# Kernel tuning notes

Measured on AMD Instinct MI355X. Metric: run time of the kernel, lower is better.

The kernel has to match this reference:

```python
import jax, jax.numpy as jnp
import numpy as np

B, C, N, OUT, K = 8, 64, 4096, 64, 20
KNN_SKIP = 6   # knn computed on channels 6: (as in x[:, 6:])
BN_EPS = 1e-5
NEG_SLOPE = 0.2


def setup_inputs() -> dict:
    key = jax.random.key(0)
    k1, k2, k3, k4 = jax.random.split(key, 4)
    x = jax.random.normal(k1, (B, C, N), dtype=jnp.float32)
    W = jax.random.normal(k2, (OUT, 2 * C), dtype=jnp.float32) * (1.0 / np.sqrt(2 * C))
    gamma = jax.random.normal(k3, (OUT,), dtype=jnp.float32) * 0.1 + 1.0
    beta = jax.random.normal(k4, (OUT,), dtype=jnp.float32) * 0.1
    return {"x": x, "W": W, "gamma": gamma, "beta": beta}


def _knn_idx(xk, k):
    # xk: (B, Ck, N). pairwise_distance[b,i,j] = -||x_i - x_j||^2
    sq = jnp.sum(xk * xk, axis=1)                       # (B, N)
    inner = jnp.einsum('bcn,bcm->bnm', xk, xk)          # (B, N, N)
    pd = 2.0 * inner - sq[:, :, None] - sq[:, None, :]  # (B, N, N)
    return jax.lax.top_k(pd, k)[1]                      # (B, N, k) int32


def reference(x, W, gamma, beta):
    idx = _knn_idx(x[:, KNN_SKIP:, :], K)               # (B, N, K)
    xt = jnp.transpose(x, (0, 2, 1))                    # (B, N, C)
    # gather neighbor features: (B, N, K, C)
    neigh = jnp.take_along_axis(xt[:, None, :, :], idx[:, :, :, None], axis=2)
    center = jnp.broadcast_to(xt[:, :, None, :], neigh.shape)
    edge = jnp.concatenate([neigh - center, center], axis=-1)  # (B, N, K, 2C)
    # 1x1 conv (no bias): contract channel dim -> (B, OUT, N, K)
    y = jnp.einsum('bnkc,oc->bonk', edge, W)
    # BatchNorm2d (training-mode batch stats, biased variance)
    mean = jnp.mean(y, axis=(0, 2, 3), keepdims=True)
    var = jnp.var(y, axis=(0, 2, 3), keepdims=True)
    y = (y - mean) * jax.lax.rsqrt(var + BN_EPS)
    y = y * gamma[None, :, None, None] + beta[None, :, None, None]
    # LeakyReLU(0.2)
    y = jnp.where(y >= 0, y, NEG_SLOPE * y)
    # max over k neighbors -> (B, OUT, N)
    return jnp.max(y, axis=-1)
```

## Files before the change

kernel.cpp:

```cpp
#include <hip/hip_runtime.h>
#include <cstdint>
#include <cstddef>

#define BB 8
#define CC 64
#define NN 4096
#define OO 64
#define KK 20
#define KC 58
#define HC 29
#define KSKIP 6
#define NSPLIT 8
#define JS 512
#define TIDX 8
#define REC 28
#define BN_EPS 1e-5f
#define NEG 0.2f
#define NEGINF (-3.402823466e38f)
#define M_TOTAL 655360.0f
#define HPAD 4

#define MED3F(a, b, c) __builtin_amdgcn_fmed3f((a), (b), (c))


__global__ void k_sq(const float* __restrict__ x, float* __restrict__ h) {
  int n = blockIdx.x * 256 + threadIdx.x;
  int b = n >> 12;
  int nn = n & (NN - 1);
  const float* xp = x + ((size_t)b * CC + KSKIP) * NN + nn;
  float s = 0.f;
#pragma unroll
  for (int c = 0; c < KC; ++c) {
    float v = xp[(size_t)c * NN];
    s = fmaf(v, v, s);
  }
  h[n] = 0.5f * s;
}

#define RIP(tv, e)                                   \
  do {                                               \
    float _e = (e);                                  \
    tv[19] = MED3F(tv[18], tv[19], _e);              \
    tv[18] = MED3F(tv[17], tv[18], _e);              \
    tv[17] = MED3F(tv[16], tv[17], _e);              \
    tv[16] = MED3F(tv[15], tv[16], _e);              \
    tv[15] = MED3F(tv[14], tv[15], _e);              \
    tv[14] = MED3F(tv[13], tv[14], _e);              \
    tv[13] = MED3F(tv[12], tv[13], _e);              \
    tv[12] = MED3F(tv[11], tv[12], _e);              \
    tv[11] = MED3F(tv[10], tv[11], _e);              \
    tv[10] = MED3F(tv[9],  tv[10], _e);              \
    tv[9]  = MED3F(tv[8],  tv[9],  _e);              \
    tv[8]  = MED3F(tv[7],  tv[8],  _e);              \
    tv[7]  = MED3F(tv[6],  tv[7],  _e);              \
    tv[6]  = MED3F(tv[5],  tv[6],  _e);              \
    tv[5]  = MED3F(tv[4],  tv[5],  _e);              \
    tv[4]  = MED3F(tv[3],  tv[4],  _e);              \
    tv[3]  = MED3F(tv[2],  tv[3],  _e);              \
    tv[2]  = MED3F(tv[1],  tv[2],  _e);              \
    tv[1]  = MED3F(tv[0],  tv[1],  _e);              \
    tv[0]  = fmaxf(tv[0], _e);                       \
  } while (0)

#define RIPX(tv, ti, e, jj)                                                   \
  do {                                                                        \
    float _e = (e);                                                           \
    int _j = (jj);                                                            \
    bool c0 = _e > tv[0], c1 = _e > tv[1], c2 = _e > tv[2], c3 = _e > tv[3];  \
    bool c4 = _e > tv[4], c5 = _e > tv[5], c6 = _e > tv[6], c7 = _e > tv[7];  \
    tv[19] = MED3F(tv[18], tv[19], _e);                                       \
    tv[18] = MED3F(tv[17], tv[18], _e);                                       \
    tv[17] = MED3F(tv[16], tv[17], _e);                                       \
    tv[16] = MED3F(tv[15], tv[16], _e);                                       \
    tv[15] = MED3F(tv[14], tv[15], _e);                                       \
    tv[14] = MED3F(tv[13], tv[14], _e);                                       \
    tv[13] = MED3F(tv[12], tv[13], _e);                                       \
    tv[12] = MED3F(tv[11], tv[12], _e);                                       \
    tv[11] = MED3F(tv[10], tv[11], _e);                                       \
    tv[10] = MED3F(tv[9],  tv[10], _e);                                       \
    tv[9]  = MED3F(tv[8],  tv[9],  _e);                                       \
    tv[8]  = MED3F(tv[7],  tv[8],  _e);                                       \
    tv[7]  = MED3F(tv[6],  tv[7],  _e); ti[7] = c6 ? ti[6] : (c7 ? _j : ti[7]); \
    tv[6]  = MED3F(tv[5],  tv[6],  _e); ti[6] = c5 ? ti[5] : (c6 ? _j : ti[6]); \
    tv[5]  = MED3F(tv[4],  tv[5],  _e); ti[5] = c4 ? ti[4] : (c5 ? _j : ti[5]); \
    tv[4]  = MED3F(tv[3],  tv[4],  _e); ti[4] = c3 ? ti[3] : (c4 ? _j : ti[4]); \
    tv[3]  = MED3F(tv[2],  tv[3],  _e); ti[3] = c2 ? ti[2] : (c3 ? _j : ti[3]); \
    tv[2]  = MED3F(tv[1],  tv[2],  _e); ti[2] = c1 ? ti[1] : (c2 ? _j : ti[2]); \
    tv[1]  = MED3F(tv[0],  tv[1],  _e); ti[1] = c0 ? ti[0] : (c1 ? _j : ti[1]); \
    tv[0]  = fmaxf(tv[0], _e);          ti[0] = c0 ? _j : ti[0];              \
  } while (0)

#define DIST8P(jq)                                                    \
  float a0 = 0.f, a1 = 0.f, a2 = 0.f, a3 = 0.f;                       \
  float a4 = 0.f, a5 = 0.f, a6 = 0.f, a7 = 0.f;                       \
  _Pragma("unroll")                                                   \
  for (int cc = 0; cc < HC; ++cc) {                                   \
    float4 x0 = *(const float4*)(ltp + cc * 64 + (jq) * 8);           \
    float4 x1 = *(const float4*)(ltp + cc * 64 + (jq) * 8 + 4);       \
    float xic = xi[cc];                                               \
    a0 = fmaf(xic, x0.x, a0); a1 = fmaf(xic, x0.y, a1);               \
    a2 = fmaf(xic, x0.z, a2); a3 = fmaf(xic, x0.w, a3);               \
    a4 = fmaf(xic, x1.x, a4); a5 = fmaf(xic, x1.y, a5);               \
    a6 = fmaf(xic, x1.z, a6); a7 = fmaf(xic, x1.w, a7);               \
  }                                                                   \
  a0 += __shfl_xor(a0, 1); a1 += __shfl_xor(a1, 1);                   \
  a2 += __shfl_xor(a2, 1); a3 += __shfl_xor(a3, 1);                   \
  a4 += __shfl_xor(a4, 1); a5 += __shfl_xor(a5, 1);                   \
  a6 += __shfl_xor(a6, 1); a7 += __shfl_xor(a7, 1);                   \
  float4 hA = *(const float4*)(lh + (jq) * 8 + half4);                \
  float d0 = (half4 ? a4 : a0) - hA.x;                                \
  float d1 = (half4 ? a5 : a1) - hA.y;                                \
  float d2 = (half4 ? a6 : a2) - hA.z;                                \
  float d3 = (half4 ? a7 : a3) - hA.w;

#define STAGE_TILE(jbase)                                             \
  __syncthreads();                                                    \
  for (int f = t; f < KC * 16; f += 256) {                            \
    int c = f >> 4, q = f & 15;                                       \
    float4 v = *(const float4*)(xb + c * NN + (jbase) + q * 4);       \
    *(float4*)(ltile + c * 64 + q * 4 + (c >= HC ? HPAD : 0)) = v;    \
  }                                                                   \
  if (t < 64) lh[t] = hg[b * NN + (jbase) + t];                       \
  __syncthreads();

__global__ __launch_bounds__(256, 4) void k_knnA(const float* __restrict__ x,
                                                 const float* __restrict__ hg,
                                                 float* __restrict__ candvx) {
  __shared__ float ltile[KC * 64 + HPAD];
  __shared__ float lh[64];
  int t = threadIdx.x;
  int l = t & 63;
  int w = t >> 6;
  int half = l & 1;
  int half4 = half * 4;
  int bidx = blockIdx.x;
  int b = bidx >> 8;
  int itile = (bidx >> 3) & 31;
  int split = bidx & 7;
  int i = itile * 128 + w * 32 + (l >> 1);
  const float* xb = x + ((size_t)b * CC + KSKIP) * NN;
  const float* ltp = ltile + half * (HC * 64 + HPAD);

  float xi[HC];
#pragma unroll
  for (int cc = 0; cc < HC; ++cc) xi[cc] = xb[(half * HC + cc) * NN + i];

  float tv[KK];
  int ti[TIDX];
#pragma unroll
  for (int s = 0; s < KK; ++s) tv[s] = NEGINF;
#pragma unroll
  for (int s = 0; s < TIDX; ++s) ti[s] = -1;

#pragma unroll 1
  for (int jt = 0; jt < JS / 64; ++jt) {
    int jbase = split * JS + jt * 64;
    STAGE_TILE(jbase)
#pragma unroll 1
    for (int jq = 0; jq < 8; ++jq) {
      DIST8P(jq)
      int j0 = jbase + jq * 8 + half4;
      RIPX(tv, ti, d0, j0 + 0); RIPX(tv, ti, d1, j0 + 1);
      RIPX(tv, ti, d2, j0 + 2); RIPX(tv, ti, d3, j0 + 3);
    }
  }

  float ov[KK];
  int oi[TIDX];
#pragma unroll
  for (int s = 0; s < KK; ++s) ov[s] = __shfl_xor(tv[s], 1);
#pragma unroll
  for (int s = 0; s < TIDX; ++s) oi[s] = __shfl_xor(ti[s], 1);
#pragma unroll
  for (int s = 0; s < TIDX; ++s) { RIPX(tv, ti, ov[s], oi[s]); }
#pragma unroll
  for (int s = TIDX; s < KK; ++s) { RIPX(tv, ti, ov[s], -1); }

  if (!half) {
    float* cv = candvx + (((size_t)(b * NN + i)) * NSPLIT + split) * REC;
    *(float4*)(cv + 0)  = make_float4(tv[0], tv[1], tv[2], tv[3]);
    *(float4*)(cv + 4)  = make_float4(tv[4], tv[5], tv[6], tv[7]);
    *(float4*)(cv + 8)  = make_float4(tv[8], tv[9], tv[10], tv[11]);
    *(float4*)(cv + 12) = make_float4(tv[12], tv[13], tv[14], tv[15]);
    *(float4*)(cv + 16) = make_float4(tv[16], tv[17], tv[18], tv[19]);
    int* cvi = (int*)(cv + KK);
    *(int4*)(cvi + 0) = make_int4(ti[0], ti[1], ti[2], ti[3]);
    *(int4*)(cvi + 4) = make_int4(ti[4], ti[5], ti[6], ti[7]);
  }
}

__global__ void k_thresh(const float* __restrict__ candvx, float* __restrict__ thr) {
  int qi = blockIdx.x * 256 + threadIdx.x;
  const float* cv = candvx + (size_t)qi * NSPLIT * REC;
  float tv[KK];
#pragma unroll
  for (int s = 0; s < KK; ++s) tv[s] = NEGINF;
#pragma unroll 1
  for (int sp = 0; sp < NSPLIT; ++sp) {
#pragma unroll
    for (int s = 0; s < KK; ++s) {
      RIP(tv, cv[sp * REC + s]);
    }
  }
  thr[qi] = tv[19];
}

__global__ void k_final(const float* __restrict__ candvx, const float* __restrict__ thr,
                        int* __restrict__ idxk, int* __restrict__ fbl,
                        int* __restrict__ fbcnt) {
  int qi = blockIdx.x * 256 + threadIdx.x;
  float ti_ = thr[qi];
  const float* cv = candvx + (size_t)qi * NSPLIT * REC;
  int* op = idxk + (size_t)qi * KK;
  bool fb = false;
  int m = 0;
#pragma unroll 1
  for (int sp = 0; sp < NSPLIT; ++sp) {
    const float* r = cv + sp * REC;
    if (r[TIDX] >= ti_) fb = true;
    const int* ri = (const int*)(r + KK);
#pragma unroll
    for (int s = 0; s < TIDX; ++s) {
      float v = r[s];
      if (v >= ti_ && ri[s] < 0) fb = true;
      if (v > ti_) {
        if (m < KK) op[m] = ri[s];
        ++m;
      }
    }
  }
  if (m >= KK) fb = true;
  if (fb) {
    int p = atomicAdd(fbcnt, 1);
    fbl[p] = qi;
    return;
  }
  int need = KK - m;
  int last = -1;
#pragma unroll 1
  for (int r2 = 0; r2 < need; ++r2) {
    int best = 0x7fffffff;
#pragma unroll 1
    for (int sp = 0; sp < NSPLIT; ++sp) {
      const float* r = cv + sp * REC;
      const int* ri = (const int*)(r + KK);
#pragma unroll
      for (int s = 0; s < TIDX; ++s) {
        if (r[s] == ti_) {
          int jx = ri[s];
          if (jx > last && jx < best) best = jx;
        }
      }
    }
    op[m + r2] = best;
    last = best;
  }
}

__global__ __launch_bounds__(256) void k_fb(const float* __restrict__ x,
                                            const float* __restrict__ hg,
                                            const float* __restrict__ thr,
                                            const int* __restrict__ fbl,
                                            const int* __restrict__ fbcnt,
                                            int* __restrict__ idxk) {
  __shared__ float xiA[HC];
  __shared__ float xiB[HC];
  __shared__ float db[64 * 2];
  __shared__ int cnt;
  int t = threadIdx.x;
  int nfb = *fbcnt;
  if (nfb > BB * NN) nfb = BB * NN;
#pragma unroll 1
  for (int q = blockIdx.x; q < nfb; q += gridDim.x) {
    int qi = fbl[q];
    int b = qi >> 12;
    int i = qi & (NN - 1);
    const float* xb = x + ((size_t)b * CC + KSKIP) * NN;
    if (t < HC) xiA[t] = xb[t * NN + i];
    else if (t < 2 * HC) xiB[t - HC] = xb[(size_t)t * NN + i];
    if (t == 0) cnt = 0;
    __syncthreads();
    float ti_ = thr[qi];
#pragma unroll 1
    for (int j = t; j < NN; j += 256) {
      float s1 = 0.f, s2 = 0.f;
#pragma unroll
      for (int cc = 0; cc < HC; ++cc) s1 = fmaf(xiA[cc], xb[cc * NN + j], s1);
#pragma unroll
      for (int cc = 0; cc < HC; ++cc) s2 = fmaf(xiB[cc], xb[(HC + cc) * NN + j], s2);
      float d = (s1 + s2) - hg[b * NN + j];
      if (d >= ti_) {
        int p = atomicAdd(&cnt, 1);
        if (p < 64) { db[p * 2] = d; db[p * 2 + 1] = __int_as_float(j); }
      }
    }
    __syncthreads();
    if (t == 0) {
      int n = cnt;
      if (n > 64) n = 64;
      int* op = idxk + (size_t)qi * KK;
      int m = 0;
      for (int e = 0; e < n; ++e) {
        if (db[e * 2] > ti_) {
          if (m < KK) op[m] = __float_as_int(db[e * 2 + 1]);
          ++m;
        }
      }
      int need = KK - m;
      int last = -1;
      for (int r = 0; r < need; ++r) {
        int best = 0x7fffffff;
        for (int e = 0; e < n; ++e) {
          if (db[e * 2] == ti_) {
            int jx = __float_as_int(db[e * 2 + 1]);
            if (jx > last && jx < best) best = jx;
          }
        }
        op[m + r] = best;
        last = best;
      }
    }
    __syncthreads();
  }
}

__global__ void k_uv(const float* __restrict__ x, const float* __restrict__ W,
                     float* __restrict__ ut, float* __restrict__ vt) {
  __shared__ float w1[64 * 65];
  __shared__ float wd[64 * 65];
  __shared__ float xs[64 * 72];
  int t = threadIdx.x;
  int b = blockIdx.x >> 6;
  int nbase = (blockIdx.x & 63) * 64;

  for (int f = t; f < 4096; f += 256) {
    int o = f >> 6, c = f & 63;
    float a = W[o * 128 + c];
    float b2 = W[o * 128 + 64 + c];
    w1[c * 65 + o] = a;
    wd[c * 65 + o] = b2 - a;
  }
  for (int f = t; f < 1024; f += 256) {
    int c = f >> 4, q = f & 15;
    float4 v = *(const float4*)(x + ((size_t)b * CC + c) * NN + nbase + q * 4);
    *(float4*)(xs + c * 72 + q * 4) = v;
  }
  __syncthreads();

  int o = t & 63, w = t >> 6;
  float4 au[4], av[4];
#pragma unroll
  for (int nq = 0; nq < 4; ++nq) {
    au[nq] = make_float4(0.f, 0.f, 0.f, 0.f);
    av[nq] = make_float4(0.f, 0.f, 0.f, 0.f);
  }
#pragma unroll 4
  for (int c = 0; c < 64; ++c) {
    float w1v = w1[c * 65 + o];
    float wdv = wd[c * 65 + o];
#pragma unroll
    for (int nq = 0; nq < 4; ++nq) {
      float4 xv = *(const float4*)(xs + c * 72 + w * 16 + nq * 4);
      au[nq].x = fmaf(w1v, xv.x, au[nq].x);
      au[nq].y = fmaf(w1v, xv.y, au[nq].y);
      au[nq].z = fmaf(w1v, xv.z, au[nq].z);
      au[nq].w = fmaf(w1v, xv.w, au[nq].w);
      av[nq].x = fmaf(wdv, xv.x, av[nq].x);
      av[nq].y = fmaf(wdv, xv.y, av[nq].y);
      av[nq].z = fmaf(wdv, xv.z, av[nq].z);
      av[nq].w = fmaf(wdv, xv.w, av[nq].w);
    }
  }
#pragma unroll
  for (int nq = 0; nq < 4; ++nq) {
    int n = nbase + w * 16 + nq * 4;
    size_t base = ((size_t)b * NN + n) * OO + o;
    ut[base + 0 * OO] = au[nq].x;
    ut[base + 1 * OO] = au[nq].y;
    ut[base + 2 * OO] = au[nq].z;
    ut[base + 3 * OO] = au[nq].w;
    vt[base + 0 * OO] = av[nq].x;
    vt[base + 1 * OO] = av[nq].y;
    vt[base + 2 * OO] = av[nq].z;
    vt[base + 3 * OO] = av[nq].w;
  }
}

__global__ void k_stats(const float* __restrict__ ut, const float* __restrict__ vt,
                        const int* __restrict__ idxk, float* __restrict__ gsum,
                        float* __restrict__ gsqs) {
  __shared__ float red[2][4][64];
  int t = threadIdx.x;
  int o = t & 63, w = t >> 6;
  int b = blockIdx.x >> 6;
  int nbase = (blockIdx.x & 63) * 64 + w * 16;
  const float* up = ut + (size_t)b * NN * OO;
  float s = 0.f, s2 = 0.f;
#pragma unroll 1
  for (int nn2 = 0; nn2 < 16; ++nn2) {
    int n = nbase + nn2;
    float vv = vt[((size_t)b * NN + n) * OO + o];
    const int* ip = idxk + ((size_t)b * NN + n) * KK;
    int4 q0 = *(const int4*)(ip + 0);
    int4 q1 = *(const int4*)(ip + 4);
    int4 q2 = *(const int4*)(ip + 8);
    int4 q3 = *(const int4*)(ip + 12);
    int4 q4 = *(const int4*)(ip + 16);
#define ACC(j)                                  \
    {                                           \
      float u = up[(size_t)(j) * OO + o];       \
      float yy = u + vv;                        \
      s += yy;                                  \
      s2 = fmaf(yy, yy, s2);                    \
    }
    ACC(q0.x) ACC(q0.y) ACC(q0.z) ACC(q0.w)
    ACC(q1.x) ACC(q1.y) ACC(q1.z) ACC(q1.w)
    ACC(q2.x) ACC(q2.y) ACC(q2.z) ACC(q2.w)
    ACC(q3.x) ACC(q3.y) ACC(q3.z) ACC(q3.w)
    ACC(q4.x) ACC(q4.y) ACC(q4.z) ACC(q4.w)
#undef ACC
  }
  red[0][w][o] = s;
  red[1][w][o] = s2;
  __syncthreads();
  if (w == 0) {
    float ts = red[0][0][o] + red[0][1][o] + red[0][2][o] + red[0][3][o];
    float t2 = red[1][0][o] + red[1][1][o] + red[1][2][o] + red[1][3][o];
    atomicAdd(&gsum[o], ts);
    atomicAdd(&gsqs[o], t2);
  }
}

__global__ void k_bn(const float* __restrict__ gsum, const float* __restrict__ gsqs,
                     const float* __restrict__ gamma, const float* __restrict__ beta,
                     float* __restrict__ AB) {
  int o = threadIdx.x;
  float mean = gsum[o] * (1.f / M_TOTAL);
  float var = gsqs[o] * (1.f / M_TOTAL) - mean * mean;
  float A = gamma[o] / sqrtf(var + BN_EPS);
  AB[o] = A;
  AB[64 + o] = beta[o] - mean * A;
}

__global__ void k_out(const float* __restrict__ ut, const float* __restrict__ vt,
                      const int* __restrict__ idxk, const float* __restrict__ AB,
                      float* __restrict__ outp) {
  __shared__ float lt[64 * 65];
  int t = threadIdx.x;
  int o = t & 63, w = t >> 6;
  int b = blockIdx.x >> 6;
  int nb = (blockIdx.x & 63) * 64;
  float A = AB[o], Bs = AB[64 + o];
  const float* up = ut + (size_t)b * NN * OO;
#pragma unroll 1
  for (int nn2 = 0; nn2 < 16; ++nn2) {
    int nl = w * 16 + nn2;
    int n = nb + nl;
    float vv = vt[((size_t)b * NN + n) * OO + o];
    const int* ip = idxk + ((size_t)b * NN + n) * KK;
    int4 q0 = *(const int4*)(ip + 0);
    int4 q1 = *(const int4*)(ip + 4);
    int4 q2 = *(const int4*)(ip + 8);
    int4 q3 = *(const int4*)(ip + 12);
    int4 q4 = *(const int4*)(ip + 16);
    float m = NEGINF;
#define STEP(j)                                   \
    {                                             \
      float u = up[(size_t)(j) * OO + o];         \
      float y = fmaf(A, u + vv, Bs);              \
      y = fmaxf(y, NEG * y);                      \
      m = fmaxf(m, y);                            \
    }
    STEP(q0.x) STEP(q0.y) STEP(q0.z) STEP(q0.w)
    STEP(q1.x) STEP(q1.y) STEP(q1.z) STEP(q1.w)
    STEP(q2.x) STEP(q2.y) STEP(q2.z) STEP(q2.w)
    STEP(q3.x) STEP(q3.y) STEP(q3.z) STEP(q3.w)
    STEP(q4.x) STEP(q4.y) STEP(q4.z) STEP(q4.w)
#undef STEP
    lt[nl * 65 + o] = m;
  }
  __syncthreads();
  int oo = t >> 2, part = t & 3;
#pragma unroll
  for (int mq = 0; mq < 4; ++mq) {
    int n0 = part * 16 + mq * 4;
    float4 vvv;
    vvv.x = lt[(n0 + 0) * 65 + oo];
    vvv.y = lt[(n0 + 1) * 65 + oo];
    vvv.z = lt[(n0 + 2) * 65 + oo];
    vvv.w = lt[(n0 + 3) * 65 + oo];
    *(float4*)(outp + ((size_t)b * OO + oo) * NN + nb + n0) = vvv;
  }
}

extern "C" void kernel_launch(void* const* d_in, const int* in_sizes, int n_in,
                              void* d_out, int out_size, void* d_ws, size_t ws_size,
                              hipStream_t stream) {
  const float* x = (const float*)d_in[0];
  const float* W = (const float*)d_in[1];
  const float* gamma = (const float*)d_in[2];
  const float* beta = (const float*)d_in[3];
  float* outp = (float*)d_out;
  char* ws = (char*)d_ws;

  const size_t NQ = (size_t)BB * NN;
  size_t off = 0;
  float* hg = (float*)(ws + off); off += NQ * 4;
  float* thr = (float*)(ws + off); off += NQ * 4;
  int* idxk = (int*)(ws + off); off += NQ * KK * 4;
  int* fbcnt = (int*)(ws + off); off += 256;
  int* fbl = (int*)(ws + off); off += NQ * 4;
  float* gsum = (float*)(ws + off); off += 256;
  float* gsqs = (float*)(ws + off); off += 256;
  float* AB = (float*)(ws + off); off += 512;
  char* region = ws + off;
  float* candvx = (float*)region;
  float* ut = (float*)region;
  float* vt = (float*)(region + NQ * OO * 4);

  k_sq<<<BB * NN / 256, 256, 0, stream>>>(x, hg);
  k_knnA<<<BB * 32 * NSPLIT, 256, 0, stream>>>(x, hg, candvx);
  k_thresh<<<BB * NN / 256, 256, 0, stream>>>(candvx, thr);
  hipMemsetAsync(fbcnt, 0, 4, stream);
  k_final<<<BB * NN / 256, 256, 0, stream>>>(candvx, thr, idxk, fbl, fbcnt);
  k_fb<<<256, 256, 0, stream>>>(x, hg, thr, fbl, fbcnt, idxk);
  k_uv<<<BB * 64, 256, 0, stream>>>(x, W, ut, vt);
  hipMemsetAsync(gsum, 0, 512, stream);
  k_stats<<<BB * 64, 256, 0, stream>>>(ut, vt, idxk, gsum, gsqs);
  k_bn<<<1, 64, 0, stream>>>(gsum, gsqs, gamma, beta, AB);
  k_out<<<BB * 64, 256, 0, stream>>>(ut, vt, idxk, AB, outp);
}
```

Measured before the change: 691.8 us.

## Track only top-8 per split in knn pass and recompute exact threshold in fallback

The per-split top-K register list in the main knn kernel shrinks from 20 values to 8, cutting the sorting-network work per candidate and halving the candidate record size. The threshold and final kernels are merged: the 20th-best value is estimated from the 8 stored per split, and a query goes to fallback whenever any split's 8th value reaches that threshold. The fallback kernel now computes the exact 20th-best distance itself, using a per-thread top-20 and a shared-memory tree reduction, before collecting neighbours. This trades a cheaper main pass for a possibly much larger fallback rate, since queries whose true neighbours cluster in one split will need a full rescan.

```diff
diff --git a/kernel.cpp b/kernel.cpp
--- a/kernel.cpp
+++ b/kernel.cpp
@@ -13,7 +13,8 @@
 #define NSPLIT 8
 #define JS 512
 #define TIDX 8
-#define REC 28
+#define REC 16
+#define FBCAP 96
 #define BN_EPS 1e-5f
 #define NEG 0.2f
 #define NEGINF (-3.402823466e38f)
@@ -62,32 +63,20 @@
     tv[0]  = fmaxf(tv[0], _e);                       \
   } while (0)
 
-#define RIPX(tv, ti, e, jj)                                                   \
+#define RIPX8(tv, ti, e, jj)                                                  \
   do {                                                                        \
     float _e = (e);                                                           \
     int _j = (jj);                                                            \
     bool c0 = _e > tv[0], c1 = _e > tv[1], c2 = _e > tv[2], c3 = _e > tv[3];  \
     bool c4 = _e > tv[4], c5 = _e > tv[5], c6 = _e > tv[6], c7 = _e > tv[7];  \
-    tv[19] = MED3F(tv[18], tv[19], _e);                                       \
-    tv[18] = MED3F(tv[17], tv[18], _e);                                       \
-    tv[17] = MED3F(tv[16], tv[17], _e);                                       \
-    tv[16] = MED3F(tv[15], tv[16], _e);                                       \
-    tv[15] = MED3F(tv[14], tv[15], _e);                                       \
-    tv[14] = MED3F(tv[13], tv[14], _e);                                       \
-    tv[13] = MED3F(tv[12], tv[13], _e);                                       \
-    tv[12] = MED3F(tv[11], tv[12], _e);                                       \
-    tv[11] = MED3F(tv[10], tv[11], _e);                                       \
-    tv[10] = MED3F(tv[9],  tv[10], _e);                                       \
-    tv[9]  = MED3F(tv[8],  tv[9],  _e);                                       \
-    tv[8]  = MED3F(tv[7],  tv[8],  _e);                                       \
-    tv[7]  = MED3F(tv[6],  tv[7],  _e); ti[7] = c6 ? ti[6] : (c7 ? _j : ti[7]); \
-    tv[6]  = MED3F(tv[5],  tv[6],  _e); ti[6] = c5 ? ti[5] : (c6 ? _j : ti[6]); \
-    tv[5]  = MED3F(tv[4],  tv[5],  _e); ti[5] = c4 ? ti[4] : (c5 ? _j : ti[5]); \
-    tv[4]  = MED3F(tv[3],  tv[4],  _e); ti[4] = c3 ? ti[3] : (c4 ? _j : ti[4]); \
-    tv[3]  = MED3F(tv[2],  tv[3],  _e); ti[3] = c2 ? ti[2] : (c3 ? _j : ti[3]); \
-    tv[2]  = MED3F(tv[1],  tv[2],  _e); ti[2] = c1 ? ti[1] : (c2 ? _j : ti[2]); \
-    tv[1]  = MED3F(tv[0],  tv[1],  _e); ti[1] = c0 ? ti[0] : (c1 ? _j : ti[1]); \
-    tv[0]  = fmaxf(tv[0], _e);          ti[0] = c0 ? _j : ti[0];              \
+    tv[7] = MED3F(tv[6], tv[7], _e); ti[7] = c6 ? ti[6] : (c7 ? _j : ti[7]);  \
+    tv[6] = MED3F(tv[5], tv[6], _e); ti[6] = c5 ? ti[5] : (c6 ? _j : ti[6]);  \
+    tv[5] = MED3F(tv[4], tv[5], _e); ti[5] = c4 ? ti[4] : (c5 ? _j : ti[5]);  \
+    tv[4] = MED3F(tv[3], tv[4], _e); ti[4] = c3 ? ti[3] : (c4 ? _j : ti[4]);  \
+    tv[3] = MED3F(tv[2], tv[3], _e); ti[3] = c2 ? ti[2] : (c3 ? _j : ti[3]);  \
+    tv[2] = MED3F(tv[1], tv[2], _e); ti[2] = c1 ? ti[1] : (c2 ? _j : ti[2]);  \
+    tv[1] = MED3F(tv[0], tv[1], _e); ti[1] = c0 ? ti[0] : (c1 ? _j : ti[1]);  \
+    tv[0] = fmaxf(tv[0], _e);        ti[0] = c0 ? _j : ti[0];                 \
   } while (0)
 
 #define DIST8P(jq)                                                    \
@@ -145,12 +134,10 @@
 #pragma unroll
   for (int cc = 0; cc < HC; ++cc) xi[cc] = xb[(half * HC + cc) * NN + i];
 
-  float tv[KK];
+  float tv[TIDX];
   int ti[TIDX];
 #pragma unroll
-  for (int s = 0; s < KK; ++s) tv[s] = NEGINF;
-#pragma unroll
-  for (int s = 0; s < TIDX; ++s) ti[s] = -1;
+  for (int s = 0; s < TIDX; ++s) { tv[s] = NEGINF; ti[s] = -1; }
 
 #pragma unroll 1
   for (int jt = 0; jt < JS / 64; ++jt) {
@@ -160,76 +147,65 @@
     for (int jq = 0; jq < 8; ++jq) {
       DIST8P(jq)
       int j0 = jbase + jq * 8 + half4;
-      RIPX(tv, ti, d0, j0 + 0); RIPX(tv, ti, d1, j0 + 1);
-      RIPX(tv, ti, d2, j0 + 2); RIPX(tv, ti, d3, j0 + 3);
-    }
-  }
-
-  float ov[KK];
+      RIPX8(tv, ti, d0, j0 + 0); RIPX8(tv, ti, d1, j0 + 1);
+      RIPX8(tv, ti, d2, j0 + 2); RIPX8(tv, ti, d3, j0 + 3);
+    }
+  }
+
+  float ov[TIDX];
   int oi[TIDX];
 #pragma unroll
-  for (int s = 0; s < KK; ++s) ov[s] = __shfl_xor(tv[s], 1);
+  for (int s = 0; s < TIDX; ++s) ov[s] = __shfl_xor(tv[s], 1);
 #pragma unroll
   for (int s = 0; s < TIDX; ++s) oi[s] = __shfl_xor(ti[s], 1);
 #pragma unroll
-  for (int s = 0; s < TIDX; ++s) { RIPX(tv, ti, ov[s], oi[s]); }
-#pragma unroll
-  for (int s = TIDX; s < KK; ++s) { RIPX(tv, ti, ov[s], -1); }
+  for (int s = 0; s < TIDX; ++s) { RIPX8(tv, ti, ov[s], oi[s]); }
 
   if (!half) {
     float* cv = candvx + (((size_t)(b * NN + i)) * NSPLIT + split) * REC;
-    *(float4*)(cv + 0)  = make_float4(tv[0], tv[1], tv[2], tv[3]);
-    *(float4*)(cv + 4)  = make_float4(tv[4], tv[5], tv[6], tv[7]);
-    *(float4*)(cv + 8)  = make_float4(tv[8], tv[9], tv[10], tv[11]);
-    *(float4*)(cv + 12) = make_float4(tv[12], tv[13], tv[14], tv[15]);
-    *(float4*)(cv + 16) = make_float4(tv[16], tv[17], tv[18], tv[19]);
-    int* cvi = (int*)(cv + KK);
+    *(float4*)(cv + 0) = make_float4(tv[0], tv[1], tv[2], tv[3]);
+    *(float4*)(cv + 4) = make_float4(tv[4], tv[5], tv[6], tv[7]);
+    int* cvi = (int*)(cv + TIDX);
     *(int4*)(cvi + 0) = make_int4(ti[0], ti[1], ti[2], ti[3]);
     *(int4*)(cvi + 4) = make_int4(ti[4], ti[5], ti[6], ti[7]);
   }
 }
 
-__global__ void k_thresh(const float* __restrict__ candvx, float* __restrict__ thr) {
+__global__ void k_final(const float* __restrict__ candvx, int* __restrict__ idxk,
+                        int* __restrict__ fbl, int* __restrict__ fbcnt) {
   int qi = blockIdx.x * 256 + threadIdx.x;
   const float* cv = candvx + (size_t)qi * NSPLIT * REC;
   float tv[KK];
 #pragma unroll
   for (int s = 0; s < KK; ++s) tv[s] = NEGINF;
-#pragma unroll 1
-  for (int sp = 0; sp < NSPLIT; ++sp) {
-#pragma unroll
-    for (int s = 0; s < KK; ++s) {
-      RIP(tv, cv[sp * REC + s]);
-    }
-  }
-  thr[qi] = tv[19];
-}
-
-__global__ void k_final(const float* __restrict__ candvx, const float* __restrict__ thr,
-                        int* __restrict__ idxk, int* __restrict__ fbl,
-                        int* __restrict__ fbcnt) {
-  int qi = blockIdx.x * 256 + threadIdx.x;
-  float ti_ = thr[qi];
-  const float* cv = candvx + (size_t)qi * NSPLIT * REC;
-  int* op = idxk + (size_t)qi * KK;
-  bool fb = false;
-  int m = 0;
+  float v7max = NEGINF;
 #pragma unroll 1
   for (int sp = 0; sp < NSPLIT; ++sp) {
     const float* r = cv + sp * REC;
-    if (r[TIDX] >= ti_) fb = true;
-    const int* ri = (const int*)(r + KK);
-#pragma unroll
-    for (int s = 0; s < TIDX; ++s) {
-      float v = r[s];
-      if (v >= ti_ && ri[s] < 0) fb = true;
-      if (v > ti_) {
-        if (m < KK) op[m] = ri[s];
-        ++m;
+#pragma unroll
+    for (int s = 0; s < TIDX; ++s) { RIP(tv, r[s]); }
+    v7max = fmaxf(v7max, r[TIDX - 1]);
+  }
+  float thr = tv[19];
+  int* op = idxk + (size_t)qi * KK;
+  int m = 0;
+  bool fb = (v7max >= thr);
+  if (!fb) {
+#pragma unroll 1
+    for (int sp = 0; sp < NSPLIT; ++sp) {
+      const float* r = cv + sp * REC;
+      const int* ri = (const int*)(r + TIDX);
+#pragma unroll
+      for (int s = 0; s < TIDX; ++s) {
+        float v = r[s];
+        if (v > thr) {
+          if (m < KK) op[m] = ri[s];
+          ++m;
+        }
       }
     }
-  }
-  if (m >= KK) fb = true;
+    if (m >= KK) fb = true;
+  }
   if (fb) {
     int p = atomicAdd(fbcnt, 1);
     fbl[p] = qi;
@@ -243,10 +219,10 @@
 #pragma unroll 1
     for (int sp = 0; sp < NSPLIT; ++sp) {
       const float* r = cv + sp * REC;
-      const int* ri = (const int*)(r + KK);
+      const int* ri = (const int*)(r + TIDX);
 #pragma unroll
       for (int s = 0; s < TIDX; ++s) {
-        if (r[s] == ti_) {
+        if (r[s] == thr) {
           int jx = ri[s];
           if (jx > last && jx < best) best = jx;
         }
@@ -259,13 +235,13 @@
 
 __global__ __launch_bounds__(256) void k_fb(const float* __restrict__ x,
                                             const float* __restrict__ hg,
-                                            const float* __restrict__ thr,
                                             const int* __restrict__ fbl,
                                             const int* __restrict__ fbcnt,
                                             int* __restrict__ idxk) {
   __shared__ float xiA[HC];
   __shared__ float xiB[HC];
-  __shared__ float db[64 * 2];
+  __shared__ float lists[256 * KK];
+  __shared__ float db[FBCAP * 2];
   __shared__ int cnt;
   int t = threadIdx.x;
   int nfb = *fbcnt;
@@ -280,7 +256,10 @@
     else if (t < 2 * HC) xiB[t - HC] = xb[(size_t)t * NN + i];
     if (t == 0) cnt = 0;
     __syncthreads();
-    float ti_ = thr[qi];
+
+    float tv[KK];
+#pragma unroll
+    for (int s = 0; s < KK; ++s) tv[s] = NEGINF;
 #pragma unroll 1
     for (int j = t; j < NN; j += 256) {
       float s1 = 0.f, s2 = 0.f;
@@ -289,19 +268,45 @@
 #pragma unroll
       for (int cc = 0; cc < HC; ++cc) s2 = fmaf(xiB[cc], xb[(HC + cc) * NN + j], s2);
       float d = (s1 + s2) - hg[b * NN + j];
-      if (d >= ti_) {
+      RIP(tv, d);
+    }
+#pragma unroll
+    for (int s = 0; s < KK; ++s) lists[t * KK + s] = tv[s];
+    __syncthreads();
+#pragma unroll 1
+    for (int st = 128; st >= 1; st >>= 1) {
+      if (t < st) {
+#pragma unroll
+        for (int s = 0; s < KK; ++s) { RIP(tv, lists[(t + st) * KK + s]); }
+#pragma unroll
+        for (int s = 0; s < KK; ++s) lists[t * KK + s] = tv[s];
+      }
+      __syncthreads();
+    }
+    float thr = lists[KK - 1];
+    __syncthreads();
+
+#pragma unroll 1
+    for (int j = t; j < NN; j += 256) {
+      float s1 = 0.f, s2 = 0.f;
+#pragma unroll
+      for (int cc = 0; cc < HC; ++cc) s1 = fmaf(xiA[cc], xb[cc * NN + j], s1);
+#pragma unroll
+      for (int cc = 0; cc < HC; ++cc) s2 = fmaf(xiB[cc], xb[(HC + cc) * NN + j], s2);
+      float d = (s1 + s2) - hg[b * NN + j];
+      if (d >= thr) {
         int p = atomicAdd(&cnt, 1);
-        if (p < 64) { db[p * 2] = d; db[p * 2 + 1] = __int_as_float(j); }
+        if (p < FBCAP) { db[p * 2] = d; db[p * 2 + 1] = __int_as_float(j); }
       }
     }
     __syncthreads();
     if (t == 0) {
       int n = cnt;
-      if (n > 64) n = 64;
+      if (n > FBCAP) n = FBCAP;
       int* op = idxk + (size_t)qi * KK;
       int m = 0;
       for (int e = 0; e < n; ++e) {
-        if (db[e * 2] > ti_) {
+        if (db[e * 2] > thr) {
           if (m < KK) op[m] = __float_as_int(db[e * 2 + 1]);
           ++m;
         }
@@ -311,7 +316,7 @@
       for (int r = 0; r < need; ++r) {
         int best = 0x7fffffff;
         for (int e = 0; e < n; ++e) {
-          if (db[e * 2] == ti_) {
+          if (db[e * 2] == thr) {
             int jx = __float_as_int(db[e * 2 + 1]);
             if (jx > last && jx < best) best = jx;
           }
@@ -506,7 +511,6 @@
   const size_t NQ = (size_t)BB * NN;
   size_t off = 0;
   float* hg = (float*)(ws + off); off += NQ * 4;
-  float* thr = (float*)(ws + off); off += NQ * 4;
   int* idxk = (int*)(ws + off); off += NQ * KK * 4;
   int* fbcnt = (int*)(ws + off); off += 256;
   int* fbl = (int*)(ws + off); off += NQ * 4;
@@ -520,10 +524,9 @@
 
   k_sq<<<BB * NN / 256, 256, 0, stream>>>(x, hg);
   k_knnA<<<BB * 32 * NSPLIT, 256, 0, stream>>>(x, hg, candvx);
-  k_thresh<<<BB * NN / 256, 256, 0, stream>>>(candvx, thr);
   hipMemsetAsync(fbcnt, 0, 4, stream);
-  k_final<<<BB * NN / 256, 256, 0, stream>>>(candvx, thr, idxk, fbl, fbcnt);
-  k_fb<<<256, 256, 0, stream>>>(x, hg, thr, fbl, fbcnt, idxk);
+  k_final<<<BB * NN / 256, 256, 0, stream>>>(candvx, idxk, fbl, fbcnt);
+  k_fb<<<256, 256, 0, stream>>>(x, hg, fbl, fbcnt, idxk);
   k_uv<<<BB * 64, 256, 0, stream>>>(x, W, ut, vt);
   hipMemsetAsync(gsum, 0, 512, stream);
   k_stats<<<BB * 64, 256, 0, stream>>>(ut, vt, idxk, gsum, gsqs);
```

After: 812.2 us. 17.4% more time.
